# Kernel optimization log

Measured on AMD Instinct MI355X. Metric: run time of the kernel, lower is better.

## Reference

```python
import jax, jax.numpy as jnp
import numpy as np

N = 100000
E = 1600000
D_IN = 128
D_H = 128
N_LAYERS = 3


def setup_inputs() -> dict:
    key = jax.random.key(0)
    ks = jax.random.split(key, 4 + 3 * N_LAYERS)
    x = jax.random.normal(ks[0], (N, D_IN), dtype=jnp.float32)
    edge_index = jax.random.randint(ks[1], (2, E), 0, N, dtype=jnp.int64)
    inp = {"x": x, "edge_index": edge_index}
    d_prev = D_IN
    for i in range(N_LAYERS):
        s = 1.0 / np.sqrt(d_prev)
        inp[f"w_rel{i}"] = jax.random.normal(ks[2 + 3 * i], (D_H, d_prev), dtype=jnp.float32) * s
        inp[f"b_rel{i}"] = jnp.zeros((D_H,), dtype=jnp.float32)
        inp[f"w_root{i}"] = jax.random.normal(ks[3 + 3 * i], (D_H, d_prev), dtype=jnp.float32) * s
        d_prev = D_H
    inp["w_out"] = jax.random.normal(ks[-2], (1, D_H), dtype=jnp.float32) / np.sqrt(D_H)
    inp["b_out"] = jnp.zeros((1,), dtype=jnp.float32)
    return inp


def _graph_conv(x, src, dst, w_rel, b_rel, w_root):
    # PyG GraphConv: out_i = W_rel @ sum_{j->i} x_j + b_rel + W_root @ x_i
    msg = x[src]                                        # [E, d] gather
    aggr = jax.ops.segment_sum(msg, dst, num_segments=N)  # [N, d] scatter-add
    return aggr @ w_rel.T + b_rel + x @ w_root.T


def reference(x, edge_index, w_rel0, b_rel0, w_root0, w_rel1, b_rel1, w_root1,
              w_rel2, b_rel2, w_root2, w_out, b_out):
    src, dst = edge_index[0], edge_index[1]
    params = [(w_rel0, b_rel0, w_root0), (w_rel1, b_rel1, w_root1), (w_rel2, b_rel2, w_root2)]
    h = x
    for w_rel, b_rel, w_root in params:
        h = jax.nn.relu(_graph_conv(h, src, dst, w_rel, b_rel, w_root))
    return h @ w_out.T + b_out  # [N, 1]
```

## Files before the change

### kernel.cpp

```cpp
#include <hip/hip_runtime.h>

constexpr int N_NODES = 100000;
constexpr int N_EDGES = 1600000;
constexpr int NPART = 8;
constexpr int PART_SZ = (N_NODES + NPART - 1) / NPART;
constexpr int CAP = 64;

typedef short short8 __attribute__((ext_vector_type(8)));
typedef float f32x4 __attribute__((ext_vector_type(4)));

__device__ __forceinline__ unsigned short f2bf(float f) {
    unsigned int u = __float_as_uint(f);
    unsigned int r = (u + 0x7fff + ((u >> 16) & 1)) >> 16;
    return (unsigned short)r;
}
__device__ __forceinline__ float bflo(unsigned int u) { return __uint_as_float(u << 16); }
__device__ __forceinline__ float bfhi(unsigned int u) { return __uint_as_float(u & 0xffff0000u); }


__global__ __launch_bounds__(256) void pack_w(const float* __restrict__ wrel,
                                              const float* __restrict__ wroot,
                                              unsigned short* __restrict__ packed) {
    int t = blockIdx.x * 256 + threadIdx.x;
    int j = t & 7, lane = (t >> 3) & 63, ks = (t >> 9) & 7, nt = (t >> 12) & 7;
    int k = ks * 32 + ((lane >> 4) << 3) + j;
    int n = nt * 16 + (lane & 15);
    float v = (k < 128) ? wrel[n * 128 + k] : wroot[n * 128 + (k - 128)];
    packed[t] = f2bf(v);
}

__global__ __launch_bounds__(256) void convert_x(const float* __restrict__ x,
                                                 unsigned short* __restrict__ A) {
    int i = blockIdx.x * 256 + threadIdx.x;
    if (i >= N_NODES * 64) return;
    int node = i >> 6, c2 = (i & 63) * 2;
    float2 v = *(const float2*)&x[(size_t)node * 128 + c2];
    unsigned int out = (unsigned int)f2bf(v.x) | ((unsigned int)f2bf(v.y) << 16);
    *(unsigned int*)&A[(size_t)node * 256 + 128 + c2] = out;
}

__global__ __launch_bounds__(256) void bucket_fill_part(const int* __restrict__ src,
                                                        const int* __restrict__ dst,
                                                        int* __restrict__ cnt,
                                                        int* __restrict__ bkt) {
    int p = blockIdx.x & 7;
    int nb = gridDim.x >> 3;
    int bi = blockIdx.x >> 3;
    int lo = p * PART_SZ, hi = lo + PART_SZ;
    for (int e = bi * 256 + threadIdx.x; e < N_EDGES; e += nb * 256) {
        int d = dst[e];
        if (d >= lo && d < hi) {
            int pos = atomicAdd(&cnt[d], 1);
            bkt[(d << 6) + pos] = src[e];
        }
    }
}

__global__ __launch_bounds__(256) void gather_bucket(const int* __restrict__ cnt_arr,
                                                     const int* __restrict__ bkt,
                                                     unsigned short* __restrict__ A) {
    int wid = (blockIdx.x * 256 + threadIdx.x) >> 6;
    int lane = threadIdx.x & 63;
    if (wid >= N_NODES) return;
    int cnt = cnt_arr[wid];
    cnt = (cnt > CAP) ? CAP : cnt;
    const int* bp = bkt + (wid << 6);
    int g = lane >> 4;
    int ch = lane & 15;
    float acc[8] = {};
    int e = 0;
    for (; e + 8 <= cnt; e += 8) {
        int s0 = bp[e + g];
        int s1 = bp[e + 4 + g];
        uint4 u0 = *(const uint4*)&A[(size_t)s0 * 256 + 128 + ch * 8];
        uint4 u1 = *(const uint4*)&A[(size_t)s1 * 256 + 128 + ch * 8];
        acc[0] += bflo(u0.x); acc[1] += bfhi(u0.x);
        acc[2] += bflo(u0.y); acc[3] += bfhi(u0.y);
        acc[4] += bflo(u0.z); acc[5] += bfhi(u0.z);
        acc[6] += bflo(u0.w); acc[7] += bfhi(u0.w);
        acc[0] += bflo(u1.x); acc[1] += bfhi(u1.x);
        acc[2] += bflo(u1.y); acc[3] += bfhi(u1.y);
        acc[4] += bflo(u1.z); acc[5] += bfhi(u1.z);
        acc[6] += bflo(u1.w); acc[7] += bfhi(u1.w);
    }
    for (; e < cnt; e += 4) {
        int ei = e + g;
        if (ei < cnt) {
            int s0 = bp[ei];
            uint4 u0 = *(const uint4*)&A[(size_t)s0 * 256 + 128 + ch * 8];
            acc[0] += bflo(u0.x); acc[1] += bfhi(u0.x);
            acc[2] += bflo(u0.y); acc[3] += bfhi(u0.y);
            acc[4] += bflo(u0.z); acc[5] += bfhi(u0.z);
            acc[6] += bflo(u0.w); acc[7] += bfhi(u0.w);
        }
    }
    #pragma unroll
    for (int j = 0; j < 8; ++j) {
        acc[j] += __shfl_xor(acc[j], 16);
        acc[j] += __shfl_xor(acc[j], 32);
    }
    if (g == 0) {
        uint4 o;
        o.x = (unsigned int)f2bf(acc[0]) | ((unsigned int)f2bf(acc[1]) << 16);
        o.y = (unsigned int)f2bf(acc[2]) | ((unsigned int)f2bf(acc[3]) << 16);
        o.z = (unsigned int)f2bf(acc[4]) | ((unsigned int)f2bf(acc[5]) << 16);
        o.w = (unsigned int)f2bf(acc[6]) | ((unsigned int)f2bf(acc[7]) << 16);
        *(uint4*)&A[(size_t)wid * 256 + ch * 8] = o;
    }
}

template <bool LAST>
__global__ __launch_bounds__(256) void mfma_transform(unsigned short* __restrict__ A,
                                                      const unsigned short* __restrict__ packedW,
                                                      const float* __restrict__ brel,
                                                      const float* __restrict__ w_out,
                                                      const float* __restrict__ b_out,
                                                      float* __restrict__ outF) {
    __shared__ unsigned short sW[32768];
    {
        const uint4* g = (const uint4*)packedW;
        uint4* s = (uint4*)sW;
        for (int i = threadIdx.x; i < 4096; i += 256) s[i] = g[i];
    }
    __syncthreads();
    int wave = threadIdx.x >> 6, lane = threadIdx.x & 63;
    int l15 = lane & 15, lhi = lane >> 4;
    int brow = blockIdx.x * 256 + wave * 64;
    float bias[8], wo[8];
    #pragma unroll
    for (int nt = 0; nt < 8; ++nt) {
        bias[nt] = brel[nt * 16 + l15];
        if (LAST) wo[nt] = w_out[nt * 16 + l15];
    }
    float bout = LAST ? b_out[0] : 0.f;

    for (int rtp = 0; rtp < 2; ++rtp) {
        int r0 = brow + rtp * 32;
        short8 a[2][8];
        #pragma unroll
        for (int rt = 0; rt < 2; ++rt) {
            int row = r0 + rt * 16 + l15;
            if (row >= N_NODES) row = N_NODES - 1;
            const unsigned short* ap = &A[(size_t)row * 256 + lhi * 8];
            #pragma unroll
            for (int ks = 0; ks < 8; ++ks) a[rt][ks] = *(const short8*)(ap + ks * 32);
        }
        f32x4 acc[2][8] = {};
        #pragma unroll
        for (int nt = 0; nt < 8; ++nt) {
            #pragma unroll
            for (int ks = 0; ks < 8; ++ks) {
                short8 b = *(const short8*)&sW[(size_t)((nt * 8 + ks) * 64 + lane) * 8];
                acc[0][nt] = __builtin_amdgcn_mfma_f32_16x16x32_bf16(a[0][ks], b, acc[0][nt], 0, 0, 0);
                acc[1][nt] = __builtin_amdgcn_mfma_f32_16x16x32_bf16(a[1][ks], b, acc[1][nt], 0, 0, 0);
            }
        }
        #pragma unroll
        for (int rt = 0; rt < 2; ++rt) {
            if (LAST) {
                #pragma unroll
                for (int rg = 0; rg < 4; ++rg) {
                    float p = 0.f;
                    #pragma unroll
                    for (int nt = 0; nt < 8; ++nt)
                        p += fmaxf(acc[rt][nt][rg] + bias[nt], 0.f) * wo[nt];
                    p += __shfl_xor(p, 1);
                    p += __shfl_xor(p, 2);
                    p += __shfl_xor(p, 4);
                    p += __shfl_xor(p, 8);
                    int row = r0 + rt * 16 + lhi * 4 + rg;
                    if (l15 == 0 && row < N_NODES) outF[row] = p + bout;
                }
            } else {
                #pragma unroll
                for (int nt = 0; nt < 8; ++nt) {
                    #pragma unroll
                    for (int rg = 0; rg < 4; ++rg) {
                        int row = r0 + rt * 16 + lhi * 4 + rg;
                        if (row < N_NODES) {
                            float v = fmaxf(acc[rt][nt][rg] + bias[nt], 0.f);
                            A[(size_t)row * 256 + 128 + nt * 16 + l15] = f2bf(v);
                        }
                    }
                }
            }
        }
    }
}

extern "C" void kernel_launch(void* const* d_in, const int* in_sizes, int n_in,
                              void* d_out, int out_size, void* d_ws, size_t ws_size,
                              hipStream_t stream) {
    const float* x      = (const float*)d_in[0];
    const int*   edge   = (const int*)d_in[1];
    const int*   src    = edge;
    const int*   dst    = edge + N_EDGES;
    const float* w_rel[3]  = {(const float*)d_in[2], (const float*)d_in[5], (const float*)d_in[8]};
    const float* b_rel[3]  = {(const float*)d_in[3], (const float*)d_in[6], (const float*)d_in[9]};
    const float* w_root[3] = {(const float*)d_in[4], (const float*)d_in[7], (const float*)d_in[10]};
    const float* w_out  = (const float*)d_in[11];
    const float* b_out  = (const float*)d_in[12];

    unsigned short* A  = (unsigned short*)d_ws;
    unsigned short* pW = A + (size_t)N_NODES * 256;
    int* cnt = (int*)(pW + 3 * 32768);
    int* bkt = cnt + N_NODES;

    for (int i = 0; i < 3; ++i)
        pack_w<<<128, 256, 0, stream>>>(w_rel[i], w_root[i], pW + (size_t)i * 32768);
    convert_x<<<(N_NODES * 64 + 255) / 256, 256, 0, stream>>>(x, A);

    hipMemsetAsync(cnt, 0, N_NODES * sizeof(int), stream);
    bucket_fill_part<<<2048, 256, 0, stream>>>(src, dst, cnt, bkt);

    const int gblocks = (N_NODES * 64 + 255) / 256;
    const int xblocks = (N_NODES + 255) / 256;

    gather_bucket<<<gblocks, 256, 0, stream>>>(cnt, bkt, A);
    mfma_transform<false><<<xblocks, 256, 0, stream>>>(A, pW + 0 * 32768, b_rel[0],
                                                       nullptr, nullptr, nullptr);
    gather_bucket<<<gblocks, 256, 0, stream>>>(cnt, bkt, A);
    mfma_transform<false><<<xblocks, 256, 0, stream>>>(A, pW + 1 * 32768, b_rel[1],
                                                       nullptr, nullptr, nullptr);
    gather_bucket<<<gblocks, 256, 0, stream>>>(cnt, bkt, A);
    mfma_transform<true><<<xblocks, 256, 0, stream>>>(A, pW + 2 * 32768, b_rel[2],
                                                      w_out, b_out, (float*)d_out);
}
```

Measured before the change: 360.0 us.

## Pre-partition edges by destination bin before bucket fill

Replaces the bucket fill, in which each of eight partition groups scanned every edge, with two passes. The first pass bins each edge into per-block, per-partition sub-buffers using shared-memory counters. The second pass has each partition's blocks read only their own bin's edges and do the atomic bucket insert. This removes the eightfold redundant reads of dst while keeping atomics local to a partition. It costs an extra kernel launch and an extra write and read of the edge pairs, and it assumes each block-bin segment never exceeds SUBCAP entries.

After: 366.1 us. About the same (+1.7%).

```diff
diff --git a/kernel.cpp b/kernel.cpp
--- a/kernel.cpp
+++ b/kernel.cpp
@@ -5,6 +5,9 @@
 constexpr int NPART = 8;
 constexpr int PART_SZ = (N_NODES + NPART - 1) / NPART;
 constexpr int CAP = 64;
+constexpr int NBLK_A = 1024;
+constexpr int EPB = (N_EDGES + NBLK_A - 1) / NBLK_A;
+constexpr int SUBCAP = 320;
 
 typedef short short8 __attribute__((ext_vector_type(8)));
 typedef float f32x4 __attribute__((ext_vector_type(4)));
@@ -39,19 +42,41 @@
     *(unsigned int*)&A[(size_t)node * 256 + 128 + c2] = out;
 }
 
-__global__ __launch_bounds__(256) void bucket_fill_part(const int* __restrict__ src,
-                                                        const int* __restrict__ dst,
-                                                        int* __restrict__ cnt,
-                                                        int* __restrict__ bkt) {
+__global__ __launch_bounds__(256) void partition_edges(const int* __restrict__ src,
+                                                       const int* __restrict__ dst,
+                                                       int2* __restrict__ binbuf,
+                                                       int* __restrict__ blkcnt) {
+    __shared__ int lc[8];
+    if (threadIdx.x < 8) lc[threadIdx.x] = 0;
+    __syncthreads();
+    int base = blockIdx.x * EPB;
+    for (int k = threadIdx.x; k < EPB; k += 256) {
+        int e = base + k;
+        if (e >= N_EDGES) break;
+        int d = __builtin_nontemporal_load(dst + e);
+        int s = __builtin_nontemporal_load(src + e);
+        int bin = d / PART_SZ;
+        int my = atomicAdd(&lc[bin], 1);
+        binbuf[(size_t)(bin * NBLK_A + blockIdx.x) * SUBCAP + my] = make_int2(d, s);
+    }
+    __syncthreads();
+    if (threadIdx.x < 8) blkcnt[blockIdx.x * 8 + threadIdx.x] = lc[threadIdx.x];
+}
+
+__global__ __launch_bounds__(256) void bucket_fill_binned(const int* __restrict__ binbuf_i,
+                                                          const int* __restrict__ blkcnt,
+                                                          int* __restrict__ cnt,
+                                                          int* __restrict__ bkt) {
     int p = blockIdx.x & 7;
-    int nb = gridDim.x >> 3;
-    int bi = blockIdx.x >> 3;
-    int lo = p * PART_SZ, hi = lo + PART_SZ;
-    for (int e = bi * 256 + threadIdx.x; e < N_EDGES; e += nb * 256) {
-        int d = dst[e];
-        if (d >= lo && d < hi) {
+    int j = blockIdx.x >> 3;
+    for (int i = j; i < NBLK_A; i += 256) {
+        int len = blkcnt[i * 8 + p];
+        const int* seg = binbuf_i + (size_t)(p * NBLK_A + i) * SUBCAP * 2;
+        for (int k = threadIdx.x; k < len; k += 256) {
+            int d = __builtin_nontemporal_load(seg + k * 2);
+            int s = __builtin_nontemporal_load(seg + k * 2 + 1);
             int pos = atomicAdd(&cnt[d], 1);
-            bkt[(d << 6) + pos] = src[e];
+            bkt[(d << 6) + pos] = s;
         }
     }
 }
@@ -203,15 +228,18 @@
 
     unsigned short* A  = (unsigned short*)d_ws;
     unsigned short* pW = A + (size_t)N_NODES * 256;
-    int* cnt = (int*)(pW + 3 * 32768);
-    int* bkt = cnt + N_NODES;
+    int* cnt    = (int*)(pW + 3 * 32768);
+    int* bkt    = cnt + N_NODES;
+    int2* binbuf = (int2*)(bkt + (size_t)N_NODES * CAP);
+    int* blkcnt = (int*)(binbuf + (size_t)NPART * NBLK_A * SUBCAP);
 
     for (int i = 0; i < 3; ++i)
         pack_w<<<128, 256, 0, stream>>>(w_rel[i], w_root[i], pW + (size_t)i * 32768);
     convert_x<<<(N_NODES * 64 + 255) / 256, 256, 0, stream>>>(x, A);
 
     hipMemsetAsync(cnt, 0, N_NODES * sizeof(int), stream);
-    bucket_fill_part<<<2048, 256, 0, stream>>>(src, dst, cnt, bkt);
+    partition_edges<<<NBLK_A, 256, 0, stream>>>(src, dst, binbuf, blkcnt);
+    bucket_fill_binned<<<2048, 256, 0, stream>>>((const int*)binbuf, blkcnt, cnt, bkt);
 
     const int gblocks = (N_NODES * 64 + 255) / 256;
     const int xblocks = (N_NODES + 255) / 256;
```

## Replace global-atomic bucket fill with two-pass binned partition and LDS bucket build

Applied to the files above, without the earlier changes.

Replaces the partitioned global-atomic bucket fill with two passes. The first pass histograms edges into 128-node bins in shared memory and reserves space per bin and block group with one global atomic per bin. It then writes packed (local dst, src) pairs into fixed-capacity segments. The second pass builds each bin's per-node buckets in LDS with shared atomics and writes them out with coalesced 16-byte stores. This removes the many scattered global atomics and the repeated 8x reads of the edge list, at the cost of extra kernels, an intermediate pairs buffer, and silent truncation if a segment overflows SEGCAP.

After: 358.1 us. About the same (-0.5%).

```diff
diff --git a/kernel.cpp b/kernel.cpp
--- a/kernel.cpp
+++ b/kernel.cpp
@@ -2,9 +2,13 @@
 
 constexpr int N_NODES = 100000;
 constexpr int N_EDGES = 1600000;
-constexpr int NPART = 8;
-constexpr int PART_SZ = (N_NODES + NPART - 1) / NPART;
 constexpr int CAP = 64;
+constexpr int NPB = 128;
+constexpr int NBIN = (N_NODES + NPB - 1) / NPB;
+constexpr int NGRP = 32;
+constexpr int SEGCAP = 128;
+constexpr int NBLK_A = 1024;
+constexpr int EPB = (N_EDGES + NBLK_A - 1) / NBLK_A;
 
 typedef short short8 __attribute__((ext_vector_type(8)));
 typedef float f32x4 __attribute__((ext_vector_type(4)));
@@ -39,20 +43,79 @@
     *(unsigned int*)&A[(size_t)node * 256 + 128 + c2] = out;
 }
 
-__global__ __launch_bounds__(256) void bucket_fill_part(const int* __restrict__ src,
-                                                        const int* __restrict__ dst,
-                                                        int* __restrict__ cnt,
-                                                        int* __restrict__ bkt) {
-    int p = blockIdx.x & 7;
-    int nb = gridDim.x >> 3;
-    int bi = blockIdx.x >> 3;
-    int lo = p * PART_SZ, hi = lo + PART_SZ;
-    for (int e = bi * 256 + threadIdx.x; e < N_EDGES; e += nb * 256) {
-        int d = dst[e];
-        if (d >= lo && d < hi) {
-            int pos = atomicAdd(&cnt[d], 1);
-            bkt[(d << 6) + pos] = src[e];
-        }
+__global__ __launch_bounds__(256) void partition_pairs(const int* __restrict__ src,
+                                                       const int* __restrict__ dst,
+                                                       int* __restrict__ gcnt,
+                                                       int* __restrict__ pairs) {
+    __shared__ int hist[NBIN];
+    __shared__ int bl[NBIN];
+    for (int j = threadIdx.x; j < NBIN; j += 256) hist[j] = 0;
+    __syncthreads();
+    int base = blockIdx.x * EPB;
+    int grp = blockIdx.x >> 5;
+    int pv[7], pr[7], pb[7];
+    bool val[7];
+    #pragma unroll
+    for (int k = 0; k < 7; ++k) {
+        int off = k * 256 + threadIdx.x;
+        int e = base + off;
+        val[k] = (off < EPB) && (e < N_EDGES);
+        pv[k] = pr[k] = pb[k] = 0;
+        if (val[k]) {
+            int d = __builtin_nontemporal_load(dst + e);
+            int s = __builtin_nontemporal_load(src + e);
+            pb[k] = d >> 7;
+            pv[k] = ((d & 127) << 17) | s;
+            pr[k] = atomicAdd(&hist[pb[k]], 1);
+        }
+    }
+    __syncthreads();
+    for (int j = threadIdx.x; j < NBIN; j += 256) {
+        int h = hist[j];
+        bl[j] = h ? atomicAdd(&gcnt[j * NGRP + grp], h) : 0;
+    }
+    __syncthreads();
+    #pragma unroll
+    for (int k = 0; k < 7; ++k)
+        if (val[k]) {
+            int idx = bl[pb[k]] + pr[k];
+            if (idx < SEGCAP)
+                pairs[((size_t)pb[k] * NGRP + grp) * SEGCAP + idx] = pv[k];
+        }
+}
+
+__global__ __launch_bounds__(256) void bucket_build(const int* __restrict__ gcnt,
+                                                    const int* __restrict__ pairs,
+                                                    int* __restrict__ cnt,
+                                                    int* __restrict__ bkt) {
+    __shared__ int cnt_l[NPB];
+    __shared__ int bkt_l[NPB * CAP];
+    int j = blockIdx.x;
+    for (int t = threadIdx.x; t < NPB; t += 256) cnt_l[t] = 0;
+    __syncthreads();
+    int wave = threadIdx.x >> 6, lane = threadIdx.x & 63;
+    for (int g = wave; g < NGRP; g += 4) {
+        int n = gcnt[j * NGRP + g];
+        n = (n > SEGCAP) ? SEGCAP : n;
+        const int* seg = pairs + ((size_t)j * NGRP + g) * SEGCAP;
+        for (int k = lane; k < n; k += 64) {
+            int p = __builtin_nontemporal_load(seg + k);
+            int dl = p >> 17;
+            int s = p & 0x1FFFF;
+            int pos = atomicAdd(&cnt_l[dl], 1);
+            if (pos < CAP) bkt_l[(dl << 6) + pos] = s;
+        }
+    }
+    __syncthreads();
+    int base_node = j * NPB;
+    for (int idx = threadIdx.x; idx < NPB * 16; idx += 256) {
+        int node = base_node + (idx >> 4);
+        if (node < N_NODES)
+            ((uint4*)bkt)[(size_t)node * 16 + (idx & 15)] = ((const uint4*)bkt_l)[idx];
+    }
+    for (int t = threadIdx.x; t < NPB; t += 256) {
+        int node = base_node + t;
+        if (node < N_NODES) cnt[node] = cnt_l[t];
     }
 }
 
@@ -203,15 +266,18 @@
 
     unsigned short* A  = (unsigned short*)d_ws;
     unsigned short* pW = A + (size_t)N_NODES * 256;
-    int* cnt = (int*)(pW + 3 * 32768);
-    int* bkt = cnt + N_NODES;
+    int* cnt   = (int*)(pW + 3 * 32768);
+    int* bkt   = cnt + N_NODES;
+    int* gcnt  = bkt + (size_t)N_NODES * CAP;
+    int* pairs = gcnt + NBIN * NGRP;
 
     for (int i = 0; i < 3; ++i)
         pack_w<<<128, 256, 0, stream>>>(w_rel[i], w_root[i], pW + (size_t)i * 32768);
     convert_x<<<(N_NODES * 64 + 255) / 256, 256, 0, stream>>>(x, A);
 
-    hipMemsetAsync(cnt, 0, N_NODES * sizeof(int), stream);
-    bucket_fill_part<<<2048, 256, 0, stream>>>(src, dst, cnt, bkt);
+    hipMemsetAsync(gcnt, 0, NBIN * NGRP * sizeof(int), stream);
+    partition_pairs<<<NBLK_A, 256, 0, stream>>>(src, dst, gcnt, pairs);
+    bucket_build<<<NBIN, 256, 0, stream>>>(gcnt, pairs, cnt, bkt);
 
     const int gblocks = (N_NODES * 64 + 255) / 256;
     const int xblocks = (N_NODES + 255) / 256;
```
